# Optimization experiments

Measured on AMD Instinct MI355X. Metric: run time of the kernel, lower is better.

Reference implementation:

```python
import jax, jax.numpy as jnp
import numpy as np

S = 72
IMG_W, IMG_H = 640, 360
STRIDE = 32
FMAP_H, FMAP_W = IMG_H // STRIDE, IMG_W // STRIDE  # 11, 20
N_OFFSETS = S
N_STRIPS = S - 1
ANGLES = np.array([15.0, 22.0, 30.0, 39.0, 49.0, 60.0, 72.0, 80.0, 90.0, 100.0, 108.0, 120.0, 131.0, 141.0, 150.0, 158.0, 165.0])
N_ANG = 17
N_PRED = 2 + 2 + 1 + N_OFFSETS  # 77
N_EDGE = FMAP_W + 2 * FMAP_H    # 42
N_PROP = N_ANG * N_EDGE         # 714
NMS_THRES = 15.0
BACKBONE_C = 512
CONV_C = 1024


def _make_anchors():
    anchor_ys = np.linspace(1.0, 0.0, N_OFFSETS)
    tan = np.tan(np.deg2rad(ANGLES))
    def side(origins):
        out = np.zeros((N_ANG, N_PRED, len(origins)), np.float32)
        for i, (sx, sy) in enumerate(origins):
            out[:, 2, i] = 1.0 - sy
            out[:, 3, i] = sx
            out[:, 5:, i] = (sx + (sy - anchor_ys)[None, :] / tan[:, None]) * IMG_W
        return out.reshape(N_ANG * N_PRED, len(origins))
    left = side([(0.0, y) for y in np.linspace(1.0, 0.0, FMAP_H)])
    right = side([(1.0, y) for y in np.linspace(1.0, 0.0, FMAP_H)])
    bottom = side([(x, 1.0) for x in np.linspace(1.0, 0.0, FMAP_W)])
    anchors = np.zeros((N_ANG * N_PRED, FMAP_H, FMAP_W), np.float32)
    anchors[:, :, 0] = left
    anchors[:, :, -1] = right
    anchors[:, -1, :] = bottom
    edge = np.concatenate([anchors[:, :, 0], anchors[:, :, -1], anchors[:, -1, :]], 1)  # [1309,42]
    anch_dim = edge.reshape(N_ANG, N_PRED, N_EDGE).transpose(2, 0, 1).reshape(N_PROP, N_PRED)
    return jnp.asarray(anchors), jnp.asarray(anch_dim)


def setup_inputs():
    key = jax.random.key(0)
    ks = jax.random.split(key, 4)
    B = 32
    feat = jax.random.normal(ks[0], (B, BACKBONE_C, FMAP_H, FMAP_W), jnp.float32)
    W_conv = jax.random.normal(ks[1], (CONV_C, BACKBONE_C), jnp.float32) * 0.02
    b_conv = jnp.zeros((CONV_C,), jnp.float32)
    W_cls = jax.random.normal(ks[2], (2 * N_ANG, CONV_C), jnp.float32) * 0.02
    b_cls = jnp.zeros((2 * N_ANG,), jnp.float32)
    W_reg = jax.random.normal(ks[3], (N_ANG * (N_OFFSETS + 1), CONV_C), jnp.float32) * 0.02
    b_reg = jnp.zeros((N_ANG * (N_OFFSETS + 1),), jnp.float32)
    anchors, anchors_anchor_dim = _make_anchors()
    return {"feat": feat, "W_conv": W_conv, "b_conv": b_conv, "W_cls": W_cls, "b_cls": b_cls,
            "W_reg": W_reg, "b_reg": b_reg, "anchors": anchors, "anchors_anchor_dim": anchors_anchor_dim}


def _proposals(feat, W_conv, b_conv, W_cls, b_cls, W_reg, b_reg, anchors):
    B = feat.shape[0]
    features = jnp.einsum('bchw,oc->bohw', feat, W_conv) + b_conv[None, :, None, None]
    cls_f = jnp.einsum('bchw,oc->bohw', features, W_cls) + b_cls[None, :, None, None]
    reg_f = jnp.einsum('bchw,oc->bohw', features, W_reg) + b_reg[None, :, None, None]
    anch = anchors.reshape(N_ANG, N_PRED, FMAP_H, FMAP_W)
    cls_r = cls_f.reshape(B, N_ANG, 2, FMAP_H, FMAP_W)
    reg_r = reg_f.reshape(B, N_ANG, N_OFFSETS + 1, FMAP_H, FMAP_W)
    # slots 0:2 <- cls logits (set), slots 2:4 <- anchor (copied), slots 4: <- anchor + reg
    mid = jnp.broadcast_to(anch[None, :, 2:4], (B, N_ANG, 2, FMAP_H, FMAP_W))
    tail = anch[None, :, 4:] + reg_r
    lane = jnp.concatenate([cls_r, mid, tail], axis=2)  # [B,17,77,h,w]
    # gather the three feature-map edges: left col, right col, bottom row
    edges = jnp.concatenate([lane[:, :, :, :, 0], lane[:, :, :, :, -1], lane[:, :, :, -1, :]], axis=3)  # [B,17,77,42]
    return edges.transpose(0, 3, 1, 2).reshape(B, N_PROP, N_PRED)  # [B,714,77]


def _nms_one(props, scores):
    # greedy line-NMS over proposals of one image, shapes static
    order = jnp.argsort(-scores)
    p = props[order]
    start = jnp.clip(jnp.round(p[:, 2] * N_STRIPS), 0.0, float(N_STRIPS))
    end = jnp.clip(start + p[:, 4] - 1.0, 0.0, float(N_STRIPS))
    xs = p[:, 5:]  # [N,72]
    s = jnp.maximum(start[:, None], start[None, :])
    e = jnp.minimum(end[:, None], end[None, :])
    idx = jnp.arange(N_OFFSETS, dtype=p.dtype)
    m = (idx[None, None, :] >= s[..., None]) & (idx[None, None, :] <= e[..., None])  # [N,N,72]
    diff = jnp.abs(xs[:, None, :] - xs[None, :, :])  # [N,N,72]
    cnt = e - s + 1.0
    dist = jnp.where(cnt > 0, jnp.sum(diff * m, -1) / jnp.maximum(cnt, 1.0), jnp.inf)
    sup = dist < NMS_THRES
    n = p.shape[0]
    pos = jnp.arange(n)
    def step(suppressed, i):
        keep_i = ~suppressed[i]
        suppressed = suppressed | (keep_i & sup[i] & (pos > i))
        return suppressed, keep_i
    _, keep_sorted = jax.lax.scan(step, jnp.zeros(n, bool), pos)
    return jnp.zeros(n, bool).at[order].set(keep_sorted)


def reference(feat, W_conv, b_conv, W_cls, b_cls, W_reg, b_reg, anchors, anchors_anchor_dim):
    proposals = _proposals(feat, W_conv, b_conv, W_cls, b_cls, W_reg, b_reg, anchors)
    scores = jax.nn.softmax(proposals[..., :2], axis=-1)[..., 1]  # [B,714]
    keep_mask = jax.lax.map(lambda pr: _nms_one(pr[0], pr[1]), (proposals, scores))  # [B,714]
    return proposals, keep_mask, scores
```

## Files before the change

### kernel.cpp

```cpp
#include <hip/hip_runtime.h>
#include <math.h>

#define NB     32
#define FH     11
#define FW     20
#define CIN    512
#define CMID   1024
#define NANG   17
#define NPREDD 77
#define NEDGE  42
#define NPROPP 714
#define NOFF   72
#define NCLS   34
#define NREGR  1241
#define N2PAD  1280
#define MTOT   1344
#define NSTRIPSF 71.0f
#define PADK   40

typedef unsigned long long u64;
typedef unsigned short ushortt;
typedef short s8v __attribute__((ext_vector_type(8)));
typedef ushortt u4v __attribute__((ext_vector_type(4)));
typedef float f4v __attribute__((ext_vector_type(4)));

__device__ inline ushortt f2bf(float f) {
    unsigned u = __float_as_uint(f);
    u += 0x7fffu + ((u >> 16) & 1u);
    return (ushortt)(u >> 16);
}
__device__ inline float bf2f(ushortt h) {
    return __uint_as_float(((unsigned)h) << 16);
}

__global__ __launch_bounds__(256) void k_prep(const float* __restrict__ feat,
                                              ushortt* __restrict__ A1hi,
                                              ushortt* __restrict__ A1lo,
                                              const float* __restrict__ Wconv,
                                              ushortt* __restrict__ B1h,
                                              ushortt* __restrict__ B1l,
                                              const float* __restrict__ Wcls,
                                              const float* __restrict__ Wreg,
                                              ushortt* __restrict__ B2h,
                                              ushortt* __restrict__ B2l)
{
    int bid = blockIdx.x, tid = threadIdx.x;
    if (bid < 2688) {
        int idx = bid * 256 + tid;
        int m = idx >> 9, c = idx & 511;
        int b = m / NEDGE, e = m - b * NEDGE;
        int h, w;
        if (e < FH)          { h = e;      w = 0;      }
        else if (e < 2 * FH) { h = e - FH; w = FW - 1; }
        else                 { h = FH - 1; w = e - 2 * FH; }
        float v = feat[((size_t)(b * CIN + c) * FH + h) * FW + w];
        ushortt hi = f2bf(v);
        A1hi[idx] = hi;
        A1lo[idx] = f2bf(v - bf2f(hi));
    } else if (bid < 2688 + 512) {
        int t = (bid - 2688) * 256 + tid;
        float4 v = *(const float4*)(Wconv + (size_t)t * 4);
        float vf[4] = {v.x, v.y, v.z, v.w};
        u4v hv, lv;
#pragma unroll
        for (int j = 0; j < 4; ++j) {
            ushortt h = f2bf(vf[j]);
            hv[j] = h;
            lv[j] = f2bf(vf[j] - bf2f(h));
        }
        *(u4v*)(B1h + (size_t)t * 4) = hv;
        *(u4v*)(B1l + (size_t)t * 4) = lv;
    } else {
        int t = (bid - 3200) * 256 + tid;
        int row = t >> 8, col = (t & 255) * 4;
        float4 v = make_float4(0.f, 0.f, 0.f, 0.f);
        if (row < NCLS)              v = *(const float4*)(Wcls + (size_t)row * CMID + col);
        else if (row < NCLS + NREGR) v = *(const float4*)(Wreg + (size_t)(row - NCLS) * CMID + col);
        float vf[4] = {v.x, v.y, v.z, v.w};
        u4v hv, lv;
#pragma unroll
        for (int j = 0; j < 4; ++j) {
            ushortt h = f2bf(vf[j]);
            hv[j] = h;
            lv[j] = f2bf(vf[j] - bf2f(h));
        }
        *(u4v*)(B2h + (size_t)t * 4) = hv;
        *(u4v*)(B2l + (size_t)t * 4) = lv;
    }
}

__global__ __launch_bounds__(256) void k_gemm1m(const ushortt* __restrict__ Ahi,
                                                const ushortt* __restrict__ Alo,
                                                const ushortt* __restrict__ Bh,
                                                const ushortt* __restrict__ Bl,
                                                const float* __restrict__ bias,
                                                ushortt* __restrict__ Chi,
                                                ushortt* __restrict__ Clo)
{
    const int K = CIN, N = CMID;
    __shared__ __align__(16) ushortt Ash[2][64 * PADK], Asl[2][64 * PADK];
    __shared__ __align__(16) ushortt Bsh[2][64 * PADK], Bsl[2][64 * PADK];
    int tid = threadIdx.x;
    int m0 = blockIdx.y * 64, n0 = blockIdx.x * 64;
    int srow = tid >> 2, sg = tid & 3;
    int lane = tid & 63, wv = tid >> 6;
    int wm = (wv & 1) * 32, wn = (wv >> 1) * 32;
    int quad = lane >> 4, l15 = lane & 15;
    int wo = srow * PADK + sg * 8;

    f4v acc[2][2];
#pragma unroll
    for (int i = 0; i < 2; ++i)
#pragma unroll
        for (int j = 0; j < 2; ++j) acc[i][j] = (f4v){0.f, 0.f, 0.f, 0.f};

    const ushortt* Ahp = Ahi + (size_t)(m0 + srow) * K + sg * 8;
    const ushortt* Alp = Alo + (size_t)(m0 + srow) * K + sg * 8;
    const ushortt* Bhp = Bh  + (size_t)(n0 + srow) * K + sg * 8;
    const ushortt* Blp = Bl  + (size_t)(n0 + srow) * K + sg * 8;

    s8v ra = *(const s8v*)Ahp;
    s8v rl = *(const s8v*)Alp;
    s8v rb = *(const s8v*)Bhp;
    s8v rc = *(const s8v*)Blp;
    *(s8v*)&Ash[0][wo] = ra;
    *(s8v*)&Asl[0][wo] = rl;
    *(s8v*)&Bsh[0][wo] = rb;
    *(s8v*)&Bsl[0][wo] = rc;
    __syncthreads();

    int buf = 0;
    for (int k0 = 0; k0 < K; k0 += 32) {
        bool more = (k0 + 32 < K);
        if (more) {
            ra = *(const s8v*)(Ahp + k0 + 32);
            rl = *(const s8v*)(Alp + k0 + 32);
            rb = *(const s8v*)(Bhp + k0 + 32);
            rc = *(const s8v*)(Blp + k0 + 32);
        }
        s8v ah[2], al[2], bh[2], bl[2];
#pragma unroll
        for (int s = 0; s < 2; ++s) {
            ah[s] = *(const s8v*)&Ash[buf][(wm + s * 16 + l15) * PADK + quad * 8];
            al[s] = *(const s8v*)&Asl[buf][(wm + s * 16 + l15) * PADK + quad * 8];
            bh[s] = *(const s8v*)&Bsh[buf][(wn + s * 16 + l15) * PADK + quad * 8];
            bl[s] = *(const s8v*)&Bsl[buf][(wn + s * 16 + l15) * PADK + quad * 8];
        }
#pragma unroll
        for (int sm = 0; sm < 2; ++sm)
#pragma unroll
            for (int sn = 0; sn < 2; ++sn) {
                acc[sm][sn] = __builtin_amdgcn_mfma_f32_16x16x32_bf16(al[sm], bl[sn], acc[sm][sn], 0, 0, 0);
                acc[sm][sn] = __builtin_amdgcn_mfma_f32_16x16x32_bf16(al[sm], bh[sn], acc[sm][sn], 0, 0, 0);
                acc[sm][sn] = __builtin_amdgcn_mfma_f32_16x16x32_bf16(ah[sm], bl[sn], acc[sm][sn], 0, 0, 0);
                acc[sm][sn] = __builtin_amdgcn_mfma_f32_16x16x32_bf16(ah[sm], bh[sn], acc[sm][sn], 0, 0, 0);
            }
        if (more) {
            *(s8v*)&Ash[buf ^ 1][wo] = ra;
            *(s8v*)&Asl[buf ^ 1][wo] = rl;
            *(s8v*)&Bsh[buf ^ 1][wo] = rb;
            *(s8v*)&Bsl[buf ^ 1][wo] = rc;
        }
        __syncthreads();
        buf ^= 1;
    }
#pragma unroll
    for (int sm = 0; sm < 2; ++sm)
#pragma unroll
        for (int sn = 0; sn < 2; ++sn)
#pragma unroll
            for (int r = 0; r < 4; ++r) {
                int m = m0 + wm + sm * 16 + quad * 4 + r;
                int n = n0 + wn + sn * 16 + l15;
                float v = acc[sm][sn][r] + bias[n];
                ushortt h = f2bf(v);
                Chi[(size_t)m * N + n] = h;
                Clo[(size_t)m * N + n] = f2bf(v - bf2f(h));
            }
}

__global__ __launch_bounds__(256) void k_gemm2m(const ushortt* __restrict__ Ahi,
                                                const ushortt* __restrict__ Alo,
                                                const ushortt* __restrict__ Bh,
                                                const ushortt* __restrict__ Bl,
                                                const float* __restrict__ bcls,
                                                const float* __restrict__ breg,
                                                float* __restrict__ C)
{
    const int K = CMID;
    __shared__ __align__(16) ushortt Ash[2][64 * PADK], Asl[2][64 * PADK];
    __shared__ __align__(16) ushortt Bsh[2][64 * PADK], Bsl[2][64 * PADK];
    int tid = threadIdx.x;
    int m0 = blockIdx.y * 64, n0 = blockIdx.x * 64;
    int srow = tid >> 2, sg = tid & 3;
    int lane = tid & 63, wv = tid >> 6;
    int wm = (wv & 1) * 32, wn = (wv >> 1) * 32;
    int quad = lane >> 4, l15 = lane & 15;
    int wo = srow * PADK + sg * 8;

    f4v acc[2][2];
#pragma unroll
    for (int i = 0; i < 2; ++i)
#pragma unroll
        for (int j = 0; j < 2; ++j) acc[i][j] = (f4v){0.f, 0.f, 0.f, 0.f};

    const ushortt* Ahp = Ahi + (size_t)(m0 + srow) * K + sg * 8;
    const ushortt* Alp = Alo + (size_t)(m0 + srow) * K + sg * 8;
    const ushortt* Bhp = Bh  + (size_t)(n0 + srow) * K + sg * 8;
    const ushortt* Blp = Bl  + (size_t)(n0 + srow) * K + sg * 8;

    s8v ra = *(const s8v*)Ahp;
    s8v rl = *(const s8v*)Alp;
    s8v rb = *(const s8v*)Bhp;
    s8v rc = *(const s8v*)Blp;
    *(s8v*)&Ash[0][wo] = ra;
    *(s8v*)&Asl[0][wo] = rl;
    *(s8v*)&Bsh[0][wo] = rb;
    *(s8v*)&Bsl[0][wo] = rc;
    __syncthreads();

    int buf = 0;
    for (int k0 = 0; k0 < K; k0 += 32) {
        bool more = (k0 + 32 < K);
        if (more) {
            ra = *(const s8v*)(Ahp + k0 + 32);
            rl = *(const s8v*)(Alp + k0 + 32);
            rb = *(const s8v*)(Bhp + k0 + 32);
            rc = *(const s8v*)(Blp + k0 + 32);
        }
        s8v ah[2], al[2], bh[2], bl[2];
#pragma unroll
        for (int s = 0; s < 2; ++s) {
            ah[s] = *(const s8v*)&Ash[buf][(wm + s * 16 + l15) * PADK + quad * 8];
            al[s] = *(const s8v*)&Asl[buf][(wm + s * 16 + l15) * PADK + quad * 8];
            bh[s] = *(const s8v*)&Bsh[buf][(wn + s * 16 + l15) * PADK + quad * 8];
            bl[s] = *(const s8v*)&Bsl[buf][(wn + s * 16 + l15) * PADK + quad * 8];
        }
#pragma unroll
        for (int sm = 0; sm < 2; ++sm)
#pragma unroll
            for (int sn = 0; sn < 2; ++sn) {
                acc[sm][sn] = __builtin_amdgcn_mfma_f32_16x16x32_bf16(al[sm], bl[sn], acc[sm][sn], 0, 0, 0);
                acc[sm][sn] = __builtin_amdgcn_mfma_f32_16x16x32_bf16(al[sm], bh[sn], acc[sm][sn], 0, 0, 0);
                acc[sm][sn] = __builtin_amdgcn_mfma_f32_16x16x32_bf16(ah[sm], bl[sn], acc[sm][sn], 0, 0, 0);
                acc[sm][sn] = __builtin_amdgcn_mfma_f32_16x16x32_bf16(ah[sm], bh[sn], acc[sm][sn], 0, 0, 0);
            }
        if (more) {
            *(s8v*)&Ash[buf ^ 1][wo] = ra;
            *(s8v*)&Asl[buf ^ 1][wo] = rl;
            *(s8v*)&Bsh[buf ^ 1][wo] = rb;
            *(s8v*)&Bsl[buf ^ 1][wo] = rc;
        }
        __syncthreads();
        buf ^= 1;
    }
#pragma unroll
    for (int sm = 0; sm < 2; ++sm)
#pragma unroll
        for (int sn = 0; sn < 2; ++sn)
#pragma unroll
            for (int r = 0; r < 4; ++r) {
                int m = m0 + wm + sm * 16 + quad * 4 + r;
                int n = n0 + wn + sn * 16 + l15;
                float bb = (n < NCLS) ? bcls[n] : ((n < NCLS + NREGR) ? breg[n - NCLS] : 0.f);
                C[(size_t)m * N2PAD + n] = acc[sm][sn][r] + bb;
            }
}

__global__ __launch_bounds__(256) void k_assemble(const float* __restrict__ C2,
                                                  const float* __restrict__ AD,
                                                  float* __restrict__ outP,
                                                  float* __restrict__ outS,
                                                  float* __restrict__ startv,
                                                  float* __restrict__ endv,
                                                  float* __restrict__ xsel)
{
    int mb = blockIdx.x;
    int b = mb / NEDGE, e = mb - b * NEDGE;
    const float* c2 = C2 + (size_t)mb * N2PAD;
    int tid = threadIdx.x;
    for (int idx = tid; idx < NANG * NPREDD; idx += 256) {
        int a = idx / NPREDD, p = idx - a * NPREDD;
        int prop = e * NANG + a;
        float v;
        if (p < 2) v = c2[a * 2 + p];
        else {
            v = AD[prop * NPREDD + p];
            if (p >= 4) v += c2[NCLS + a * 73 + (p - 4)];
        }
        outP[((size_t)b * NPROPP + prop) * NPREDD + p] = v;
    }
    if (tid < NANG) {
        int a = tid, prop = e * NANG + a;
        float c0 = c2[2 * a], c1 = c2[2 * a + 1];
        float mx = fmaxf(c0, c1);
        float e0 = expf(c0 - mx), e1 = expf(c1 - mx);
        outS[b * NPROPP + prop] = e1 / (e0 + e1);
        float p2 = AD[prop * NPREDD + 2];
        float p4 = AD[prop * NPREDD + 4] + c2[NCLS + a * 73];
        float st = fminf(fmaxf(rintf(p2 * NSTRIPSF), 0.0f), NSTRIPSF);
        float en = fminf(fmaxf(st + p4 - 1.0f, 0.0f), NSTRIPSF);
        startv[b * 720 + prop] = st;
        endv[b * 720 + prop] = en;
        int ksi = (int)st;
        xsel[b * 720 + prop] = AD[prop * NPREDD + 5 + ksi] + c2[NCLS + a * 73 + ksi + 1];
    }
}

__global__ __launch_bounds__(128) void k_sort(const float* __restrict__ scores,
                                              int* __restrict__ order)
{
    int b = blockIdx.x, tile = blockIdx.y, tid = threadIdx.x;
    __shared__ __align__(16) float s[720];
    for (int x = tid; x < 720; x += 128)
        s[x] = (x < NPROPP) ? scores[b * NPROPP + x] : -1e30f;
    __syncthreads();
    int i = tile * 128 + tid;
    if (i >= NPROPP) return;
    float si = s[i];
    int r = 0;
#pragma unroll 4
    for (int j4 = 0; j4 < 720; j4 += 4) {
        float4 v = *(const float4*)&s[j4];
        r += (v.x > si) || (v.x == si && (j4 + 0) < i);
        r += (v.y > si) || (v.y == si && (j4 + 1) < i);
        r += (v.z > si) || (v.z == si && (j4 + 2) < i);
        r += (v.w > si) || (v.w == si && (j4 + 3) < i);
    }
    order[b * 720 + r] = i;
}

__global__ __launch_bounds__(256) void k_supmat(const float* __restrict__ outP,
                                                const float* __restrict__ startv,
                                                const float* __restrict__ endv,
                                                const float* __restrict__ xsel,
                                                const int* __restrict__ order,
                                                u64* __restrict__ sup)
{
    int jt = blockIdx.x, it = blockIdx.y, b = blockIdx.z;
    int i0 = it * 64, j0 = jt * 64;
    int tid = threadIdx.x;
    if (j0 + 63 < i0) {
        if (tid < 64) {
            int il = i0 + tid;
            if (il < NPROPP) sup[((size_t)b * NPROPP + il) * 12 + jt] = 0ull;
        }
        return;
    }
    __shared__ float SI[64], EI[64], XI[64];
    __shared__ float SJ[64], EJ[64], XJ[64];
    __shared__ int   OI[64], OJ[64];
    if (tid < 128) {
        int side = tid >> 6, q = tid & 63;
        int pos = (side ? j0 : i0) + q;
        int o = (pos < NPROPP) ? order[b * 720 + pos] : -1;
        float st = (o >= 0) ? startv[b * 720 + o] : 0.f;
        float en = (o >= 0) ? endv[b * 720 + o] : -2.f;
        float xv = (o >= 0) ? xsel[b * 720 + o] : 0.f;
        if (!side) { SI[q] = st; EI[q] = en; XI[q] = xv; OI[q] = o; }
        else       { SJ[q] = st; EJ[q] = en; XJ[q] = xv; OJ[q] = o; }
    }
    __syncthreads();
    int lane = tid & 63, w = tid >> 6;
    int j = j0 + lane;
    float sj = SJ[lane], ej = EJ[lane], xj = XJ[lane];
    const float* basexs = outP + (size_t)b * NPROPP * NPREDD + 5;
#pragma unroll 1
    for (int rep = 0; rep < 16; ++rep) {
        int iloc = w * 16 + rep;
        int il = i0 + iloc;
        float si = SI[iloc], ei = EI[iloc];
        float s = fmaxf(si, sj), e = fminf(ei, ej);
        float cnt = e - s + 1.0f;
        bool sp = false;
        if (cnt > 0.f) {
            if (e < s) {
                sp = true;
            } else {
                int ks = (int)s, ke = (int)e;
                if (si == sj && ke == ks) {
                    sp = (fabsf(XI[iloc] - xj) / fmaxf(cnt, 1.0f)) < 15.0f;
                } else {
                    const float* xi  = basexs + (size_t)OI[iloc] * NPREDD;
                    const float* xjp = basexs + (size_t)OJ[lane] * NPREDD;
                    float sum = 0.f;
                    for (int k = ks; k <= ke; ++k)
                        sum += fabsf(xi[k] - xjp[k]);
                    sp = (sum / fmaxf(cnt, 1.0f)) < 15.0f;
                }
            }
        }
        bool valid = (il < NPROPP) && (j < NPROPP) && (j > il);
        u64 msk = __ballot(valid && sp);
        if (lane == 0 && il < NPROPP)
            sup[((size_t)b * NPROPP + il) * 12 + jt] = msk;
    }
}

__global__ __launch_bounds__(256) void k_scan(const u64* __restrict__ sup,
                                              const int* __restrict__ order,
                                              float* __restrict__ keep_out)
{
    int b = blockIdx.x, tid = threadIdx.x;
    int lane = tid & 63;
    __shared__ u64 K[12], NS[12];
    __shared__ int changed;
    const u64* base = sup + (size_t)b * NPROPP * 12;

    int r0 = tid, r1 = tid + 256, r2 = tid + 512;
    u64 row0[12], row1[12], row2[12];
#pragma unroll
    for (int t = 0; t < 12; ++t) {
        row0[t] = base[(size_t)r0 * 12 + t];
        row1[t] = (r1 < NPROPP) ? base[(size_t)r1 * 12 + t] : 0ull;
        row2[t] = (r2 < NPROPP) ? base[(size_t)r2 * 12 + t] : 0ull;
    }
    if (tid < 12) {
        K[tid] = (tid < 11) ? ~0ull : ((1ull << (NPROPP - 704)) - 1ull);
        NS[tid] = 0ull;
    }
    __syncthreads();

    for (int sweep = 0; sweep < 720; ++sweep) {
        u64 m0 = 0ull - ((K[r0 >> 6] >> (r0 & 63)) & 1ull);
        u64 m1 = (r1 < NPROPP) ? (0ull - ((K[r1 >> 6] >> (r1 & 63)) & 1ull)) : 0ull;
        u64 m2 = (r2 < NPROPP) ? (0ull - ((K[r2 >> 6] >> (r2 & 63)) & 1ull)) : 0ull;
        unsigned lo[12], hi[12];
#pragma unroll
        for (int t = 0; t < 12; ++t) {
            u64 a = (row0[t] & m0) | (row1[t] & m1) | (row2[t] & m2);
            lo[t] = (unsigned)a;
            hi[t] = (unsigned)(a >> 32);
        }
#pragma unroll
        for (int s = 1; s < 64; s <<= 1) {
#pragma unroll
            for (int t = 0; t < 12; ++t) {
                lo[t] |= __shfl_xor(lo[t], s, 64);
                hi[t] |= __shfl_xor(hi[t], s, 64);
            }
        }
        if (tid == 0) changed = 0;
        if (lane == 0) {
#pragma unroll
            for (int t = 0; t < 12; ++t)
                atomicOr(&NS[t], ((u64)hi[t] << 32) | (u64)lo[t]);
        }
        __syncthreads();
        if (tid < 12) {
            u64 valid = (tid < 11) ? ~0ull : ((1ull << (NPROPP - 704)) - 1ull);
            u64 nk = valid & ~NS[tid];
            if (nk != K[tid]) changed = 1;
            K[tid] = nk;
            NS[tid] = 0ull;
        }
        __syncthreads();
        if (!changed) break;
    }
    if (r0 < NPROPP)
        keep_out[b * NPROPP + order[b * 720 + r0]] =
            ((K[r0 >> 6] >> (r0 & 63)) & 1ull) ? 1.f : 0.f;
    if (r1 < NPROPP)
        keep_out[b * NPROPP + order[b * 720 + r1]] =
            ((K[r1 >> 6] >> (r1 & 63)) & 1ull) ? 1.f : 0.f;
    if (r2 < NPROPP)
        keep_out[b * NPROPP + order[b * 720 + r2]] =
            ((K[r2 >> 6] >> (r2 & 63)) & 1ull) ? 1.f : 0.f;
}

extern "C" void kernel_launch(void* const* d_in, const int* in_sizes, int n_in,
                              void* d_out, int out_size, void* d_ws, size_t ws_size,
                              hipStream_t stream)
{
    const float* feat  = (const float*)d_in[0];
    const float* Wconv = (const float*)d_in[1];
    const float* bconv = (const float*)d_in[2];
    const float* Wcls  = (const float*)d_in[3];
    const float* bcls  = (const float*)d_in[4];
    const float* Wreg  = (const float*)d_in[5];
    const float* breg  = (const float*)d_in[6];
    const float* AD    = (const float*)d_in[8];

    float* out  = (float*)d_out;
    float* outP = out;
    float* outK = out + (size_t)NB * NPROPP * NPREDD;
    float* outS = outK + (size_t)NB * NPROPP;

    float* ws = (float*)d_ws;
    ushortt* A1hi = (ushortt*)ws;
    ushortt* A1lo = (ushortt*)(ws + 344064);
    ushortt* A2hi = (ushortt*)(ws + 688128);
    ushortt* A2lo = (ushortt*)(ws + 1376256);
    float*   C2   = ws + 2064384;
    ushortt* B1h  = (ushortt*)(ws + 3784704);
    ushortt* B1l  = (ushortt*)(ws + 4046848);
    ushortt* B2h  = (ushortt*)(ws + 4308992);
    ushortt* B2l  = (ushortt*)(ws + 4964352);
    float* startv = ws;
    float* endv   = ws + 23040;
    int*   order  = (int*)(ws + 46080);
    u64*   sup    = (u64*)(ws + 69120);
    float* xsel   = ws + 617472;

    k_prep        <<<dim3(4480),       dim3(256), 0, stream>>>(feat, A1hi, A1lo,
                                                               Wconv, B1h, B1l,
                                                               Wcls, Wreg, B2h, B2l);
    k_gemm1m      <<<dim3(16, 21),     dim3(256), 0, stream>>>(A1hi, A1lo, B1h, B1l, bconv, A2hi, A2lo);
    k_gemm2m      <<<dim3(20, 21),     dim3(256), 0, stream>>>(A2hi, A2lo, B2h, B2l, bcls, breg, C2);
    k_assemble    <<<dim3(MTOT),       dim3(256), 0, stream>>>(C2, AD, outP, outS, startv, endv, xsel);
    k_sort        <<<dim3(NB, 6),      dim3(128), 0, stream>>>(outS, order);
    k_supmat      <<<dim3(12, 12, NB), dim3(256), 0, stream>>>(outP, startv, endv, xsel, order, sup);
    k_scan        <<<dim3(NB),         dim3(256), 0, stream>>>(sup, order, outK);
}
```

Before: 185.0 us.

## Fuse proposal assembly into GEMM2 epilogue and drop lo*lo MFMA term

Removes the separate assemble kernel and the intermediate C2 buffer by writing proposals, softmax scores, start/end and selected x directly from the second GEMM's epilogue. The static anchor columns and per-proposal start strip are written from extra blocks in the prep kernel. Both GEMMs also drop the lo*lo bf16 MFMA product, cutting a quarter of the matrix work at a small precision cost. The epilogue now does scattered global writes and integer divisions per element.

```diff
diff --git a/kernel.cpp b/kernel.cpp
--- a/kernel.cpp
+++ b/kernel.cpp
@@ -42,7 +42,10 @@
                                               const float* __restrict__ Wcls,
                                               const float* __restrict__ Wreg,
                                               ushortt* __restrict__ B2h,
-                                              ushortt* __restrict__ B2l)
+                                              ushortt* __restrict__ B2l,
+                                              const float* __restrict__ AD,
+                                              float* __restrict__ outP,
+                                              float* __restrict__ kst)
 {
     int bid = blockIdx.x, tid = threadIdx.x;
     if (bid < 2688) {
@@ -70,7 +73,7 @@
         }
         *(u4v*)(B1h + (size_t)t * 4) = hv;
         *(u4v*)(B1l + (size_t)t * 4) = lv;
-    } else {
+    } else if (bid < 4480) {
         int t = (bid - 3200) * 256 + tid;
         int row = t >> 8, col = (t & 255) * 4;
         float4 v = make_float4(0.f, 0.f, 0.f, 0.f);
@@ -86,6 +89,19 @@
         }
         *(u4v*)(B2h + (size_t)t * 4) = hv;
         *(u4v*)(B2l + (size_t)t * 4) = lv;
+    } else if (bid < 4659) {
+        int idx = (bid - 4480) * 256 + tid;
+        if (idx < NB * NPROPP * 2) {
+            int bp = idx >> 1;
+            int p = 2 + (idx & 1);
+            int prop = bp - (bp / NPROPP) * NPROPP;
+            outP[(size_t)bp * NPREDD + p] = AD[prop * NPREDD + p];
+        }
+    } else {
+        if (tid < NPROPP) {
+            float p2 = AD[tid * NPREDD + 2];
+            kst[tid] = fminf(fmaxf(rintf(p2 * NSTRIPSF), 0.0f), NSTRIPSF);
+        }
     }
 }
 
@@ -150,7 +166,6 @@
         for (int sm = 0; sm < 2; ++sm)
 #pragma unroll
             for (int sn = 0; sn < 2; ++sn) {
-                acc[sm][sn] = __builtin_amdgcn_mfma_f32_16x16x32_bf16(al[sm], bl[sn], acc[sm][sn], 0, 0, 0);
                 acc[sm][sn] = __builtin_amdgcn_mfma_f32_16x16x32_bf16(al[sm], bh[sn], acc[sm][sn], 0, 0, 0);
                 acc[sm][sn] = __builtin_amdgcn_mfma_f32_16x16x32_bf16(ah[sm], bl[sn], acc[sm][sn], 0, 0, 0);
                 acc[sm][sn] = __builtin_amdgcn_mfma_f32_16x16x32_bf16(ah[sm], bh[sn], acc[sm][sn], 0, 0, 0);
@@ -185,7 +200,13 @@
                                                 const ushortt* __restrict__ Bl,
                                                 const float* __restrict__ bcls,
                                                 const float* __restrict__ breg,
-                                                float* __restrict__ C)
+                                                const float* __restrict__ AD,
+                                                const float* __restrict__ kst,
+                                                float* __restrict__ outP,
+                                                float* __restrict__ outS,
+                                                float* __restrict__ startv,
+                                                float* __restrict__ endv,
+                                                float* __restrict__ xsel)
 {
     const int K = CMID;
     __shared__ __align__(16) ushortt Ash[2][64 * PADK], Asl[2][64 * PADK];
@@ -240,7 +261,6 @@
         for (int sm = 0; sm < 2; ++sm)
 #pragma unroll
             for (int sn = 0; sn < 2; ++sn) {
-                acc[sm][sn] = __builtin_amdgcn_mfma_f32_16x16x32_bf16(al[sm], bl[sn], acc[sm][sn], 0, 0, 0);
                 acc[sm][sn] = __builtin_amdgcn_mfma_f32_16x16x32_bf16(al[sm], bh[sn], acc[sm][sn], 0, 0, 0);
                 acc[sm][sn] = __builtin_amdgcn_mfma_f32_16x16x32_bf16(ah[sm], bl[sn], acc[sm][sn], 0, 0, 0);
                 acc[sm][sn] = __builtin_amdgcn_mfma_f32_16x16x32_bf16(ah[sm], bh[sn], acc[sm][sn], 0, 0, 0);
@@ -254,6 +274,7 @@
         __syncthreads();
         buf ^= 1;
     }
+
 #pragma unroll
     for (int sm = 0; sm < 2; ++sm)
 #pragma unroll
@@ -262,49 +283,36 @@
             for (int r = 0; r < 4; ++r) {
                 int m = m0 + wm + sm * 16 + quad * 4 + r;
                 int n = n0 + wn + sn * 16 + l15;
-                float bb = (n < NCLS) ? bcls[n] : ((n < NCLS + NREGR) ? breg[n - NCLS] : 0.f);
-                C[(size_t)m * N2PAD + n] = acc[sm][sn][r] + bb;
+                int b = m / NEDGE, e = m - b * NEDGE;
+                bool isCls = (n < NCLS);
+                bool isReg = (n >= NCLS) && (n < NCLS + NREGR);
+                int q = n - NCLS;
+                int a = isCls ? (n >> 1) : (q / 73);
+                int p = isCls ? (n & 1) : (q - a * 73 + 4);
+                int prop = e * NANG + a;
+                float bb = isCls ? bcls[n] : (isReg ? breg[q] : 0.f);
+                float t = acc[sm][sn][r] + bb;
+                float tp = __shfl_xor(t, 1);
+                float v = t;
+                if (isReg) v = AD[(size_t)prop * NPREDD + p] + t;
+                if (isCls || isReg)
+                    outP[((size_t)b * NPROPP + prop) * NPREDD + p] = v;
+                if (isCls && !(n & 1)) {
+                    float mx = fmaxf(t, tp);
+                    float e0 = expf(t - mx), e1 = expf(tp - mx);
+                    outS[b * NPROPP + prop] = e1 / (e0 + e1);
+                }
+                if (isReg) {
+                    float stf = kst[prop];
+                    if (p == 4) {
+                        float en = fminf(fmaxf(stf + v - 1.0f, 0.0f), NSTRIPSF);
+                        startv[b * 720 + prop] = stf;
+                        endv[b * 720 + prop] = en;
+                    }
+                    if (p == 5 + (int)stf)
+                        xsel[b * 720 + prop] = v;
+                }
             }
-}
-
-__global__ __launch_bounds__(256) void k_assemble(const float* __restrict__ C2,
-                                                  const float* __restrict__ AD,
-                                                  float* __restrict__ outP,
-                                                  float* __restrict__ outS,
-                                                  float* __restrict__ startv,
-                                                  float* __restrict__ endv,
-                                                  float* __restrict__ xsel)
-{
-    int mb = blockIdx.x;
-    int b = mb / NEDGE, e = mb - b * NEDGE;
-    const float* c2 = C2 + (size_t)mb * N2PAD;
-    int tid = threadIdx.x;
-    for (int idx = tid; idx < NANG * NPREDD; idx += 256) {
-        int a = idx / NPREDD, p = idx - a * NPREDD;
-        int prop = e * NANG + a;
-        float v;
-        if (p < 2) v = c2[a * 2 + p];
-        else {
-            v = AD[prop * NPREDD + p];
-            if (p >= 4) v += c2[NCLS + a * 73 + (p - 4)];
-        }
-        outP[((size_t)b * NPROPP + prop) * NPREDD + p] = v;
-    }
-    if (tid < NANG) {
-        int a = tid, prop = e * NANG + a;
-        float c0 = c2[2 * a], c1 = c2[2 * a + 1];
-        float mx = fmaxf(c0, c1);
-        float e0 = expf(c0 - mx), e1 = expf(c1 - mx);
-        outS[b * NPROPP + prop] = e1 / (e0 + e1);
-        float p2 = AD[prop * NPREDD + 2];
-        float p4 = AD[prop * NPREDD + 4] + c2[NCLS + a * 73];
-        float st = fminf(fmaxf(rintf(p2 * NSTRIPSF), 0.0f), NSTRIPSF);
-        float en = fminf(fmaxf(st + p4 - 1.0f, 0.0f), NSTRIPSF);
-        startv[b * 720 + prop] = st;
-        endv[b * 720 + prop] = en;
-        int ksi = (int)st;
-        xsel[b * 720 + prop] = AD[prop * NPREDD + 5 + ksi] + c2[NCLS + a * 73 + ksi + 1];
-    }
 }
 
 __global__ __launch_bounds__(128) void k_sort(const float* __restrict__ scores,
@@ -491,7 +499,7 @@
     ushortt* A1lo = (ushortt*)(ws + 344064);
     ushortt* A2hi = (ushortt*)(ws + 688128);
     ushortt* A2lo = (ushortt*)(ws + 1376256);
-    float*   C2   = ws + 2064384;
+    float*   kst  = ws + 2064384;
     ushortt* B1h  = (ushortt*)(ws + 3784704);
     ushortt* B1l  = (ushortt*)(ws + 4046848);
     ushortt* B2h  = (ushortt*)(ws + 4308992);
@@ -502,12 +510,13 @@
     u64*   sup    = (u64*)(ws + 69120);
     float* xsel   = ws + 617472;
 
-    k_prep        <<<dim3(4480),       dim3(256), 0, stream>>>(feat, A1hi, A1lo,
+    k_prep        <<<dim3(4660),       dim3(256), 0, stream>>>(feat, A1hi, A1lo,
                                                                Wconv, B1h, B1l,
-                                                               Wcls, Wreg, B2h, B2l);
+                                                               Wcls, Wreg, B2h, B2l,
+                                                               AD, outP, kst);
     k_gemm1m      <<<dim3(16, 21),     dim3(256), 0, stream>>>(A1hi, A1lo, B1h, B1l, bconv, A2hi, A2lo);
-    k_gemm2m      <<<dim3(20, 21),     dim3(256), 0, stream>>>(A2hi, A2lo, B2h, B2l, bcls, breg, C2);
-    k_assemble    <<<dim3(MTOT),       dim3(256), 0, stream>>>(C2, AD, outP, outS, startv, endv, xsel);
+    k_gemm2m      <<<dim3(20, 21),     dim3(256), 0, stream>>>(A2hi, A2lo, B2h, B2l, bcls, breg,
+                                                               AD, kst, outP, outS, startv, endv, xsel);
     k_sort        <<<dim3(NB, 6),      dim3(128), 0, stream>>>(outS, order);
     k_supmat      <<<dim3(12, 12, NB), dim3(256), 0, stream>>>(outP, startv, endv, xsel, order, sup);
     k_scan        <<<dim3(NB),         dim3(256), 0, stream>>>(sup, order, outK);
```

After: 201.3 us. +8.8%, slower.
